# Kernel tuning notes

Hardware: AMD Instinct MI355X
Metric: run time of the kernel (lower is better)

## Reference

```python
import jax, jax.numpy as jnp
import numpy as np

N, B, E = 10000, 4, 160000
C_IN, C_OUT, C_E = 64, 64, 16


def _mk_params(key, c_in, c_out, c_e):
    ks = jax.random.split(key, 8)
    s = 0.1
    return dict(
        w_n=jax.random.normal(ks[0], (c_in, c_out), jnp.float32) * s,
        w_e=jax.random.normal(ks[1], (c_e, c_out), jnp.float32) * s,
        q=jax.random.normal(ks[2], (c_out, c_out), jnp.float32) * s,
        k=jax.random.normal(ks[3], (c_out, c_out), jnp.float32) * s,
        aw=jax.random.normal(ks[4], (3 * c_out, 1), jnp.float32) * s,
        ab=jax.random.normal(ks[5], (1,), jnp.float32) * s,
        ow=jax.random.normal(ks[6], (2 * c_out, c_out), jnp.float32) * s,
        ob=jax.random.normal(ks[7], (c_out,), jnp.float32) * s,
    )


def setup_inputs() -> dict:
    key = jax.random.key(0)
    kx, ke, ka, k1, k2 = jax.random.split(key, 5)
    inp = {
        'X': jax.random.normal(kx, (N, B, C_IN), jnp.float32),
        'edge_index': jax.random.randint(ke, (2, E), 0, N, jnp.int32),
        'edge_attr': jax.random.normal(ka, (E, C_E), jnp.float32),
    }
    p1 = _mk_params(k1, C_IN, C_OUT, C_E)
    p2 = _mk_params(k2, C_OUT, C_OUT, C_E)
    for name, v in p1.items():
        inp[name + '1'] = v
    for name, v in p2.items():
        inp[name + '2'] = v
    return inp


def egnn_conv(x, edge_index, edge_attr, w_n, w_e, q, k, aw, ab, ow, ob, n_nodes):
    # x: [N,B,Cin]; edge_attr: [E,Ce]
    xp = x @ w_n                         # [N,B,C]
    ea = edge_attr @ w_e                 # [E,C]
    src, dst = edge_index[0], edge_index[1]
    xj = xp[src]                         # [E,B,C] gather (source)
    xi = xp[dst]                         # [E,B,C] gather (target)
    qf = xj @ q                          # [E,B,C]
    kf = xi @ k                          # [E,B,C]
    eab = jnp.broadcast_to(ea[:, None, :], qf.shape)  # [E,B,C]
    att_feat = jnp.concatenate([qf, kf, eab], axis=-1)  # [E,B,3C]
    att = jax.nn.sigmoid(att_feat @ aw + ab)            # [E,B,1]
    gate = jax.nn.sigmoid(eab)
    msg = att * xj * gate                # [E,B,C]
    aggr = jax.ops.segment_max(msg, dst, num_segments=n_nodes)  # [N,B,C]
    aggr = jnp.where(jnp.isneginf(aggr), 0.0, aggr)  # empty segments -> 0
    out = jnp.concatenate([xp, aggr], axis=-1) @ ow + ob
    return xp + out


def reference(X, edge_index, edge_attr,
              w_n1, w_e1, q1, k1, aw1, ab1, ow1, ob1,
              w_n2, w_e2, q2, k2, aw2, ab2, ow2, ob2):
    n_nodes = X.shape[0]
    c1 = egnn_conv(X, edge_index, edge_attr, w_n1, w_e1, q1, k1, aw1, ab1, ow1, ob1, n_nodes)
    c1 = jax.nn.leaky_relu(c1, 0.01)
    c2 = egnn_conv(c1, edge_index, edge_attr, w_n2, w_e2, q2, k2, aw2, ab2, ow2, ob2, n_nodes)
    c2 = jax.nn.leaky_relu(c2, 0.01)
    return c2
```

## Files before the change

kernel.cpp:

```cpp
#include <hip/hip_runtime.h>
#include <math.h>

#define NN 10000
#define BB 4
#define EE 160000
#define CC 64
#define CE 16

static constexpr size_t OFF_XPA    = 0;
static constexpr size_t OFF_XPB    = 10240000;
static constexpr size_t OFF_SA     = 20480000;
static constexpr size_t OFF_SB     = 20640000;
static constexpr size_t OFF_VECS   = 20800000;
static constexpr size_t OFF_COUNTS = 20801280;
static constexpr size_t OFF_CURSOR = 20841280;
static constexpr size_t OFF_OFFS   = 20881280;
static constexpr size_t OFF_RECS   = 20921344;
static constexpr size_t OFF_ATT    = 22201344;

__device__ __forceinline__ float sigmoidf_(float x) {
    return 1.0f / (1.0f + __expf(-x));
}

__global__ void hist_vecs_kernel(const int* __restrict__ ei, int* __restrict__ counts,
                                 const float* __restrict__ q1, const float* __restrict__ k1,
                                 const float* __restrict__ aw1, const float* __restrict__ we1,
                                 const float* __restrict__ q2, const float* __restrict__ k2,
                                 const float* __restrict__ aw2, const float* __restrict__ we2,
                                 float* __restrict__ vecs) {
    int e = blockIdx.x * blockDim.x + threadIdx.x;
    if (e < EE) atomicAdd(&counts[ei[EE + e]], 1);
    if (blockIdx.x == 0) {
        int t = threadIdx.x;
        if (t < 64) {
            float a = 0.f, b = 0.f, c = 0.f, d = 0.f;
            for (int j = 0; j < 64; ++j) {
                a = fmaf(q1[t * 64 + j], aw1[j], a);
                b = fmaf(k1[t * 64 + j], aw1[64 + j], b);
                c = fmaf(q2[t * 64 + j], aw2[j], c);
                d = fmaf(k2[t * 64 + j], aw2[64 + j], d);
            }
            vecs[t] = a; vecs[64 + t] = b; vecs[144 + t] = c; vecs[208 + t] = d;
        }
        if (t < 16) {
            float a = 0.f, b = 0.f;
            for (int j = 0; j < 64; ++j) {
                a = fmaf(we1[t * 64 + j], aw1[128 + j], a);
                b = fmaf(we2[t * 64 + j], aw2[128 + j], b);
            }
            vecs[128 + t] = a; vecs[272 + t] = b;
        }
    }
}

__global__ void scan_kernel(const int* __restrict__ counts, int* __restrict__ offs, int n) {
    __shared__ int sm[1024];
    __shared__ int carry_s;
    int t = threadIdx.x;
    if (t == 0) carry_s = 0;
    __syncthreads();
    for (int base = 0; base < n; base += 1024) {
        int i = base + t;
        int v = (i < n) ? counts[i] : 0;
        sm[t] = v;
        __syncthreads();
        for (int off = 1; off < 1024; off <<= 1) {
            int add = (t >= off) ? sm[t - off] : 0;
            __syncthreads();
            sm[t] += add;
            __syncthreads();
        }
        int carry = carry_s;
        if (i < n) offs[i] = carry + sm[t] - v;
        __syncthreads();
        if (t == 1023) carry_s = carry + sm[1023];
        __syncthreads();
    }
    if (t == 0) offs[n] = carry_s;
}

__global__ void scatter_kernel(const int* __restrict__ ei, const int* __restrict__ offs,
                               int* __restrict__ cursor, int2* __restrict__ recs) {
    int e = blockIdx.x * blockDim.x + threadIdx.x;
    if (e >= EE) return;
    int s = ei[e], d = ei[EE + e];
    int p = atomicAdd(&cursor[d], 1);
    recs[offs[d] + p] = make_int2(s, e);
}

__global__ __launch_bounds__(256) void node_prep_kernel(
    const float* __restrict__ x,
    const float* __restrict__ w_n,
    const float* __restrict__ qa,
    const float* __restrict__ ka,
    float* __restrict__ xp,
    float* __restrict__ sa,
    float* __restrict__ sb) {
    __shared__ float w_sh[64 * 64];
    __shared__ float x_sh[4 * BB * CC];
    int t = threadIdx.x;
    for (int i = t; i < 64 * 64; i += 256) w_sh[i] = w_n[i];
    int node0 = blockIdx.x * 4;
    const float4* xg = (const float4*)(x + (size_t)node0 * BB * CC);
    ((float4*)x_sh)[t] = xg[t];
    __syncthreads();
    int wave = t >> 6, lane = t & 63;
    int node = node0 + wave;
    const float* xrow = x_sh + wave * BB * CC;
    float acc0 = 0.f, acc1 = 0.f, acc2 = 0.f, acc3 = 0.f;
    #pragma unroll 8
    for (int ci = 0; ci < 64; ++ci) {
        float w = w_sh[ci * 64 + lane];
        acc0 = fmaf(xrow[ci], w, acc0);
        acc1 = fmaf(xrow[64 + ci], w, acc1);
        acc2 = fmaf(xrow[128 + ci], w, acc2);
        acc3 = fmaf(xrow[192 + ci], w, acc3);
    }
    size_t obase = (size_t)node * BB * CC + lane;
    xp[obase] = acc0;
    xp[obase + 64] = acc1;
    xp[obase + 128] = acc2;
    xp[obase + 192] = acc3;
    float qv = qa[lane], kv = ka[lane];
    float ra0 = acc0 * qv, ra1 = acc1 * qv, ra2 = acc2 * qv, ra3 = acc3 * qv;
    float rb0 = acc0 * kv, rb1 = acc1 * kv, rb2 = acc2 * kv, rb3 = acc3 * kv;
    #pragma unroll
    for (int off = 32; off >= 1; off >>= 1) {
        ra0 += __shfl_xor(ra0, off, 64); ra1 += __shfl_xor(ra1, off, 64);
        ra2 += __shfl_xor(ra2, off, 64); ra3 += __shfl_xor(ra3, off, 64);
        rb0 += __shfl_xor(rb0, off, 64); rb1 += __shfl_xor(rb1, off, 64);
        rb2 += __shfl_xor(rb2, off, 64); rb3 += __shfl_xor(rb3, off, 64);
    }
    if (lane == 0) {
        sa[node * BB + 0] = ra0; sa[node * BB + 1] = ra1;
        sa[node * BB + 2] = ra2; sa[node * BB + 3] = ra3;
        sb[node * BB + 0] = rb0; sb[node * BB + 1] = rb1;
        sb[node * BB + 2] = rb2; sb[node * BB + 3] = rb3;
    }
}

__global__ __launch_bounds__(256) void att_kernel(
    const int* __restrict__ ei, const float* __restrict__ attr,
    const float* __restrict__ sa, const float* __restrict__ sb,
    const float* __restrict__ weav,
    const float* __restrict__ ab,
    float4* __restrict__ att) {
    int e = blockIdx.x * blockDim.x + threadIdx.x;
    if (e >= EE) return;
    int s = ei[e], d = ei[EE + e];
    const float4* ap = (const float4*)(attr + (size_t)e * CE);
    float4 a0 = ap[0], a1 = ap[1], a2 = ap[2], a3 = ap[3];
    float se = ab[0];
    se = fmaf(a0.x, weav[0], se);  se = fmaf(a0.y, weav[1], se);
    se = fmaf(a0.z, weav[2], se);  se = fmaf(a0.w, weav[3], se);
    se = fmaf(a1.x, weav[4], se);  se = fmaf(a1.y, weav[5], se);
    se = fmaf(a1.z, weav[6], se);  se = fmaf(a1.w, weav[7], se);
    se = fmaf(a2.x, weav[8], se);  se = fmaf(a2.y, weav[9], se);
    se = fmaf(a2.z, weav[10], se); se = fmaf(a2.w, weav[11], se);
    se = fmaf(a3.x, weav[12], se); se = fmaf(a3.y, weav[13], se);
    se = fmaf(a3.z, weav[14], se); se = fmaf(a3.w, weav[15], se);
    float4 sas = *(const float4*)(sa + (size_t)s * BB);
    float4 sbn = *(const float4*)(sb + (size_t)d * BB);
    float4 r;
    r.x = sigmoidf_(sas.x + sbn.x + se);
    r.y = sigmoidf_(sas.y + sbn.y + se);
    r.z = sigmoidf_(sas.z + sbn.z + se);
    r.w = sigmoidf_(sas.w + sbn.w + se);
    att[e] = r;
}

__global__ __launch_bounds__(256) void conv_out_kernel(
    const float* __restrict__ xp,
    const int2* __restrict__ recs,
    const int* __restrict__ offs,
    const float* __restrict__ attr,
    const float* __restrict__ w_e,
    const float4* __restrict__ att,
    const float* __restrict__ ow,
    const float* __restrict__ ob,
    float* __restrict__ out) {
    __shared__ float aggr_sh[4][BB * CC];
    __shared__ float xpn_sh[4][BB * CC];
    int t = threadIdx.x;
    int wave = t >> 6, lane = t & 63;
    int node = blockIdx.x * 4 + wave;

    float wec[CE];
    #pragma unroll
    for (int j = 0; j < CE; ++j) wec[j] = w_e[j * CC + lane];

    const float* xn = xp + (size_t)node * BB * CC + lane;
    float xn0 = xn[0], xn1 = xn[64], xn2 = xn[128], xn3 = xn[192];

    int o0 = offs[node], o1 = offs[node + 1];
    float m0 = -INFINITY, m1 = -INFINITY, m2 = -INFINITY, m3 = -INFINITY;

    int i = o0;
    int2 rec = (i < o1) ? recs[i] : make_int2(0, 0);
    while (i < o1) {
        int2 cur = rec;
        ++i;
        if (i < o1) rec = recs[i];
        int s = cur.x, e = cur.y;
        float4 at = att[e];
        const float4* ap = (const float4*)(attr + (size_t)e * CE);
        float4 a0 = ap[0], a1 = ap[1], a2 = ap[2], a3 = ap[3];
        float g = 0.f;
        g = fmaf(a0.x, wec[0], g);  g = fmaf(a0.y, wec[1], g);
        g = fmaf(a0.z, wec[2], g);  g = fmaf(a0.w, wec[3], g);
        g = fmaf(a1.x, wec[4], g);  g = fmaf(a1.y, wec[5], g);
        g = fmaf(a1.z, wec[6], g);  g = fmaf(a1.w, wec[7], g);
        g = fmaf(a2.x, wec[8], g);  g = fmaf(a2.y, wec[9], g);
        g = fmaf(a2.z, wec[10], g); g = fmaf(a2.w, wec[11], g);
        g = fmaf(a3.x, wec[12], g); g = fmaf(a3.y, wec[13], g);
        g = fmaf(a3.z, wec[14], g); g = fmaf(a3.w, wec[15], g);
        g = sigmoidf_(g);
        const float* xs = xp + (size_t)s * BB * CC + lane;
        float x0 = xs[0], x1 = xs[64], x2 = xs[128], x3 = xs[192];
        m0 = fmaxf(m0, at.x * x0 * g);
        m1 = fmaxf(m1, at.y * x1 * g);
        m2 = fmaxf(m2, at.z * x2 * g);
        m3 = fmaxf(m3, at.w * x3 * g);
    }
    m0 = (m0 == -INFINITY) ? 0.f : m0;
    m1 = (m1 == -INFINITY) ? 0.f : m1;
    m2 = (m2 == -INFINITY) ? 0.f : m2;
    m3 = (m3 == -INFINITY) ? 0.f : m3;

    aggr_sh[wave][0 * CC + lane] = m0; aggr_sh[wave][1 * CC + lane] = m1;
    aggr_sh[wave][2 * CC + lane] = m2; aggr_sh[wave][3 * CC + lane] = m3;
    xpn_sh[wave][0 * CC + lane] = xn0; xpn_sh[wave][1 * CC + lane] = xn1;
    xpn_sh[wave][2 * CC + lane] = xn2; xpn_sh[wave][3 * CC + lane] = xn3;
    __syncthreads();

    const float* xr = xpn_sh[wave];
    const float* ar = aggr_sh[wave];
    float o0f = 0.f, o1f = 0.f, o2f = 0.f, o3f = 0.f;
    #pragma unroll 4
    for (int ci = 0; ci < 64; ++ci) {
        float wa = ow[ci * 64 + lane];
        float wb = ow[(64 + ci) * 64 + lane];
        o0f = fmaf(xr[ci], wa, o0f);
        o1f = fmaf(xr[CC + ci], wa, o1f);
        o2f = fmaf(xr[2 * CC + ci], wa, o2f);
        o3f = fmaf(xr[3 * CC + ci], wa, o3f);
        o0f = fmaf(ar[ci], wb, o0f);
        o1f = fmaf(ar[CC + ci], wb, o1f);
        o2f = fmaf(ar[2 * CC + ci], wb, o2f);
        o3f = fmaf(ar[3 * CC + ci], wb, o3f);
    }
    float obv = ob[lane];
    float r0 = xn0 + o0f + obv;
    float r1 = xn1 + o1f + obv;
    float r2 = xn2 + o2f + obv;
    float r3 = xn3 + o3f + obv;
    r0 = (r0 > 0.f) ? r0 : 0.01f * r0;
    r1 = (r1 > 0.f) ? r1 : 0.01f * r1;
    r2 = (r2 > 0.f) ? r2 : 0.01f * r2;
    r3 = (r3 > 0.f) ? r3 : 0.01f * r3;
    float* op = out + (size_t)node * BB * CC + lane;
    op[0] = r0; op[64] = r1; op[128] = r2; op[192] = r3;
}

extern "C" void kernel_launch(void* const* d_in, const int* in_sizes, int n_in,
                              void* d_out, int out_size, void* d_ws, size_t ws_size,
                              hipStream_t stream) {
    const float* X    = (const float*)d_in[0];
    const int*   ei   = (const int*)d_in[1];
    const float* attr = (const float*)d_in[2];
    const float* w_n1 = (const float*)d_in[3];
    const float* w_e1 = (const float*)d_in[4];
    const float* q1   = (const float*)d_in[5];
    const float* k1   = (const float*)d_in[6];
    const float* aw1  = (const float*)d_in[7];
    const float* ab1  = (const float*)d_in[8];
    const float* ow1  = (const float*)d_in[9];
    const float* ob1  = (const float*)d_in[10];
    const float* w_n2 = (const float*)d_in[11];
    const float* w_e2 = (const float*)d_in[12];
    const float* q2   = (const float*)d_in[13];
    const float* k2   = (const float*)d_in[14];
    const float* aw2  = (const float*)d_in[15];
    const float* ab2  = (const float*)d_in[16];
    const float* ow2  = (const float*)d_in[17];
    const float* ob2  = (const float*)d_in[18];
    float* out = (float*)d_out;

    char* ws = (char*)d_ws;
    float*  xpA    = (float*)(ws + OFF_XPA);
    float*  xpB    = (float*)(ws + OFF_XPB);
    float*  sa     = (float*)(ws + OFF_SA);
    float*  sb     = (float*)(ws + OFF_SB);
    float*  vecs   = (float*)(ws + OFF_VECS);
    int*    counts = (int*)(ws + OFF_COUNTS);
    int*    cursor = (int*)(ws + OFF_CURSOR);
    int*    offs   = (int*)(ws + OFF_OFFS);
    int2*   recs   = (int2*)(ws + OFF_RECS);
    float4* att    = (float4*)(ws + OFF_ATT);

    hipMemsetAsync(counts, 0, 2 * NN * sizeof(int), stream);
    hist_vecs_kernel<<<EE / 256, 256, 0, stream>>>(ei, counts, q1, k1, aw1, w_e1,
                                                   q2, k2, aw2, w_e2, vecs);
    scan_kernel<<<1, 1024, 0, stream>>>(counts, offs, NN);
    scatter_kernel<<<EE / 256, 256, 0, stream>>>(ei, offs, cursor, recs);

    node_prep_kernel<<<NN / 4, 256, 0, stream>>>(X, w_n1, vecs + 0, vecs + 64, xpA, sa, sb);
    att_kernel<<<EE / 256, 256, 0, stream>>>(ei, attr, sa, sb, vecs + 128, ab1, att);
    conv_out_kernel<<<NN / 4, 256, 0, stream>>>(xpA, recs, offs, attr, w_e1, att,
                                                ow1, ob1, xpB);
    node_prep_kernel<<<NN / 4, 256, 0, stream>>>(xpB, w_n2, vecs + 144, vecs + 208, xpA, sa, sb);
    att_kernel<<<EE / 256, 256, 0, stream>>>(ei, attr, sa, sb, vecs + 272, ab2, att);
    conv_out_kernel<<<NN / 4, 256, 0, stream>>>(xpA, recs, offs, attr, w_e2, att,
                                                ow2, ob2, out);
}
```

Before: 312.8 us.

## Interleave batch into per-channel float4 layout, split aggregation from output GEMM, shuffle-based scan

Node features are now stored channel-major with the four batch values packed together, so each lane fetches a source node's features in one float4 load during the gather-max. The fused conv_out kernel is split into an aggregation kernel that writes to a new workspace buffer and a separate output projection kernel. This adds an extra round trip through global memory and an extra launch per layer. The single-block scan now uses wavefront shuffles in place of a shared-memory Hillis-Steele loop, which cuts the number of barriers.

```diff
diff --git a/kernel.cpp b/kernel.cpp
--- a/kernel.cpp
+++ b/kernel.cpp
@@ -9,14 +9,15 @@
 
 static constexpr size_t OFF_XPA    = 0;
 static constexpr size_t OFF_XPB    = 10240000;
-static constexpr size_t OFF_SA     = 20480000;
-static constexpr size_t OFF_SB     = 20640000;
-static constexpr size_t OFF_VECS   = 20800000;
-static constexpr size_t OFF_COUNTS = 20801280;
-static constexpr size_t OFF_CURSOR = 20841280;
-static constexpr size_t OFF_OFFS   = 20881280;
-static constexpr size_t OFF_RECS   = 20921344;
-static constexpr size_t OFF_ATT    = 22201344;
+static constexpr size_t OFF_AGG    = 20480000;
+static constexpr size_t OFF_SA     = 30720000;
+static constexpr size_t OFF_SB     = 30880000;
+static constexpr size_t OFF_VECS   = 31040000;
+static constexpr size_t OFF_COUNTS = 31041280;
+static constexpr size_t OFF_CURSOR = 31081280;
+static constexpr size_t OFF_OFFS   = 31121280;
+static constexpr size_t OFF_RECS   = 31161344;
+static constexpr size_t OFF_ATT    = 32441344;
 
 __device__ __forceinline__ float sigmoidf_(float x) {
     return 1.0f / (1.0f + __expf(-x));
@@ -54,29 +55,43 @@
 }
 
 __global__ void scan_kernel(const int* __restrict__ counts, int* __restrict__ offs, int n) {
-    __shared__ int sm[1024];
-    __shared__ int carry_s;
+    __shared__ int wsum[16];
+    __shared__ int carry_sh;
     int t = threadIdx.x;
-    if (t == 0) carry_s = 0;
+    int lane = t & 63, wid = t >> 6;
+    if (t == 0) carry_sh = 0;
     __syncthreads();
     for (int base = 0; base < n; base += 1024) {
         int i = base + t;
         int v = (i < n) ? counts[i] : 0;
-        sm[t] = v;
+        int x = v;
+        #pragma unroll
+        for (int d = 1; d < 64; d <<= 1) {
+            int y = __shfl_up(x, d, 64);
+            if (lane >= d) x += y;
+        }
+        if (lane == 63) wsum[wid] = x;
         __syncthreads();
-        for (int off = 1; off < 1024; off <<= 1) {
-            int add = (t >= off) ? sm[t - off] : 0;
-            __syncthreads();
-            sm[t] += add;
-            __syncthreads();
+        if (wid == 0 && lane < 16) {
+            int s = wsum[lane];
+            int y2 = s;
+            #pragma unroll
+            for (int d = 1; d < 16; d <<= 1) {
+                int z = __shfl_up(y2, d, 16);
+                if (lane >= d) y2 += z;
+            }
+            wsum[lane] = y2;
         }
-        int carry = carry_s;
-        if (i < n) offs[i] = carry + sm[t] - v;
         __syncthreads();
-        if (t == 1023) carry_s = carry + sm[1023];
+        int waveExcl = (wid == 0) ? 0 : wsum[wid - 1];
+        int carry = carry_sh;
+        if (i < n) offs[i] = carry + waveExcl + x - v;
+        int total = wsum[15];
         __syncthreads();
-    }
-    if (t == 0) offs[n] = carry_s;
+        if (t == 0) carry_sh = carry + total;
+        __syncthreads();
+    }
+    if (threadIdx.x == 0) offs[n] = carry_sh;
 }
 
 __global__ void scatter_kernel(const int* __restrict__ ei, const int* __restrict__ offs,
@@ -88,12 +103,13 @@
     recs[offs[d] + p] = make_int2(s, e);
 }
 
+template <bool IN_T>
 __global__ __launch_bounds__(256) void node_prep_kernel(
     const float* __restrict__ x,
     const float* __restrict__ w_n,
     const float* __restrict__ qa,
     const float* __restrict__ ka,
-    float* __restrict__ xp,
+    float* __restrict__ xp_t,
     float* __restrict__ sa,
     float* __restrict__ sb) {
     __shared__ float w_sh[64 * 64];
@@ -111,16 +127,17 @@
     #pragma unroll 8
     for (int ci = 0; ci < 64; ++ci) {
         float w = w_sh[ci * 64 + lane];
-        acc0 = fmaf(xrow[ci], w, acc0);
-        acc1 = fmaf(xrow[64 + ci], w, acc1);
-        acc2 = fmaf(xrow[128 + ci], w, acc2);
-        acc3 = fmaf(xrow[192 + ci], w, acc3);
-    }
-    size_t obase = (size_t)node * BB * CC + lane;
-    xp[obase] = acc0;
-    xp[obase + 64] = acc1;
-    xp[obase + 128] = acc2;
-    xp[obase + 192] = acc3;
+        float x0 = IN_T ? xrow[ci * 4 + 0] : xrow[ci];
+        float x1 = IN_T ? xrow[ci * 4 + 1] : xrow[64 + ci];
+        float x2 = IN_T ? xrow[ci * 4 + 2] : xrow[128 + ci];
+        float x3 = IN_T ? xrow[ci * 4 + 3] : xrow[192 + ci];
+        acc0 = fmaf(x0, w, acc0);
+        acc1 = fmaf(x1, w, acc1);
+        acc2 = fmaf(x2, w, acc2);
+        acc3 = fmaf(x3, w, acc3);
+    }
+    float4 st; st.x = acc0; st.y = acc1; st.z = acc2; st.w = acc3;
+    *(float4*)(xp_t + (size_t)node * 256 + lane * 4) = st;
     float qv = qa[lane], kv = ka[lane];
     float ra0 = acc0 * qv, ra1 = acc1 * qv, ra2 = acc2 * qv, ra3 = acc3 * qv;
     float rb0 = acc0 * kv, rb1 = acc1 * kv, rb2 = acc2 * kv, rb3 = acc3 * kv;
@@ -169,18 +186,14 @@
     att[e] = r;
 }
 
-__global__ __launch_bounds__(256) void conv_out_kernel(
-    const float* __restrict__ xp,
+__global__ __launch_bounds__(256) void aggr_kernel(
+    const float* __restrict__ xp_t,
     const int2* __restrict__ recs,
     const int* __restrict__ offs,
     const float* __restrict__ attr,
     const float* __restrict__ w_e,
     const float4* __restrict__ att,
-    const float* __restrict__ ow,
-    const float* __restrict__ ob,
-    float* __restrict__ out) {
-    __shared__ float aggr_sh[4][BB * CC];
-    __shared__ float xpn_sh[4][BB * CC];
+    float* __restrict__ aggr_t) {
     int t = threadIdx.x;
     int wave = t >> 6, lane = t & 63;
     int node = blockIdx.x * 4 + wave;
@@ -188,9 +201,6 @@
     float wec[CE];
     #pragma unroll
     for (int j = 0; j < CE; ++j) wec[j] = w_e[j * CC + lane];
-
-    const float* xn = xp + (size_t)node * BB * CC + lane;
-    float xn0 = xn[0], xn1 = xn[64], xn2 = xn[128], xn3 = xn[192];
 
     int o0 = offs[node], o1 = offs[node + 1];
     float m0 = -INFINITY, m1 = -INFINITY, m2 = -INFINITY, m3 = -INFINITY;
@@ -203,6 +213,7 @@
         if (i < o1) rec = recs[i];
         int s = cur.x, e = cur.y;
         float4 at = att[e];
+        float4 xv = *(const float4*)(xp_t + (size_t)s * 256 + lane * 4);
         const float4* ap = (const float4*)(attr + (size_t)e * CE);
         float4 a0 = ap[0], a1 = ap[1], a2 = ap[2], a3 = ap[3];
         float g = 0.f;
@@ -215,51 +226,72 @@
         g = fmaf(a3.x, wec[12], g); g = fmaf(a3.y, wec[13], g);
         g = fmaf(a3.z, wec[14], g); g = fmaf(a3.w, wec[15], g);
         g = sigmoidf_(g);
-        const float* xs = xp + (size_t)s * BB * CC + lane;
-        float x0 = xs[0], x1 = xs[64], x2 = xs[128], x3 = xs[192];
-        m0 = fmaxf(m0, at.x * x0 * g);
-        m1 = fmaxf(m1, at.y * x1 * g);
-        m2 = fmaxf(m2, at.z * x2 * g);
-        m3 = fmaxf(m3, at.w * x3 * g);
+        m0 = fmaxf(m0, at.x * xv.x * g);
+        m1 = fmaxf(m1, at.y * xv.y * g);
+        m2 = fmaxf(m2, at.z * xv.z * g);
+        m3 = fmaxf(m3, at.w * xv.w * g);
     }
     m0 = (m0 == -INFINITY) ? 0.f : m0;
     m1 = (m1 == -INFINITY) ? 0.f : m1;
     m2 = (m2 == -INFINITY) ? 0.f : m2;
     m3 = (m3 == -INFINITY) ? 0.f : m3;
-
-    aggr_sh[wave][0 * CC + lane] = m0; aggr_sh[wave][1 * CC + lane] = m1;
-    aggr_sh[wave][2 * CC + lane] = m2; aggr_sh[wave][3 * CC + lane] = m3;
-    xpn_sh[wave][0 * CC + lane] = xn0; xpn_sh[wave][1 * CC + lane] = xn1;
-    xpn_sh[wave][2 * CC + lane] = xn2; xpn_sh[wave][3 * CC + lane] = xn3;
+    float4 st; st.x = m0; st.y = m1; st.z = m2; st.w = m3;
+    *(float4*)(aggr_t + (size_t)node * 256 + lane * 4) = st;
+}
+
+template <bool WRITE_T>
+__global__ __launch_bounds__(256) void out_kernel(
+    const float* __restrict__ xp_t,
+    const float* __restrict__ aggr_t,
+    const float* __restrict__ ow,
+    const float* __restrict__ ob,
+    float* __restrict__ out) {
+    __shared__ float xs[4][BB * CC];
+    __shared__ float as_[4][BB * CC];
+    int t = threadIdx.x;
+    int wave = t >> 6, lane = t & 63;
+    int node = blockIdx.x * 4 + wave;
+
+    float4 xv = *(const float4*)(xp_t + (size_t)node * 256 + lane * 4);
+    float4 av = *(const float4*)(aggr_t + (size_t)node * 256 + lane * 4);
+    xs[wave][0 * 64 + lane] = xv.x; xs[wave][1 * 64 + lane] = xv.y;
+    xs[wave][2 * 64 + lane] = xv.z; xs[wave][3 * 64 + lane] = xv.w;
+    as_[wave][0 * 64 + lane] = av.x; as_[wave][1 * 64 + lane] = av.y;
+    as_[wave][2 * 64 + lane] = av.z; as_[wave][3 * 64 + lane] = av.w;
     __syncthreads();
 
-    const float* xr = xpn_sh[wave];
-    const float* ar = aggr_sh[wave];
+    const float* xr = xs[wave];
+    const float* ar = as_[wave];
     float o0f = 0.f, o1f = 0.f, o2f = 0.f, o3f = 0.f;
     #pragma unroll 4
     for (int ci = 0; ci < 64; ++ci) {
         float wa = ow[ci * 64 + lane];
         float wb = ow[(64 + ci) * 64 + lane];
         o0f = fmaf(xr[ci], wa, o0f);
-        o1f = fmaf(xr[CC + ci], wa, o1f);
-        o2f = fmaf(xr[2 * CC + ci], wa, o2f);
-        o3f = fmaf(xr[3 * CC + ci], wa, o3f);
+        o1f = fmaf(xr[64 + ci], wa, o1f);
+        o2f = fmaf(xr[128 + ci], wa, o2f);
+        o3f = fmaf(xr[192 + ci], wa, o3f);
         o0f = fmaf(ar[ci], wb, o0f);
-        o1f = fmaf(ar[CC + ci], wb, o1f);
-        o2f = fmaf(ar[2 * CC + ci], wb, o2f);
-        o3f = fmaf(ar[3 * CC + ci], wb, o3f);
+        o1f = fmaf(ar[64 + ci], wb, o1f);
+        o2f = fmaf(ar[128 + ci], wb, o2f);
+        o3f = fmaf(ar[192 + ci], wb, o3f);
     }
     float obv = ob[lane];
-    float r0 = xn0 + o0f + obv;
-    float r1 = xn1 + o1f + obv;
-    float r2 = xn2 + o2f + obv;
-    float r3 = xn3 + o3f + obv;
+    float r0 = xv.x + o0f + obv;
+    float r1 = xv.y + o1f + obv;
+    float r2 = xv.z + o2f + obv;
+    float r3 = xv.w + o3f + obv;
     r0 = (r0 > 0.f) ? r0 : 0.01f * r0;
     r1 = (r1 > 0.f) ? r1 : 0.01f * r1;
     r2 = (r2 > 0.f) ? r2 : 0.01f * r2;
     r3 = (r3 > 0.f) ? r3 : 0.01f * r3;
-    float* op = out + (size_t)node * BB * CC + lane;
-    op[0] = r0; op[64] = r1; op[128] = r2; op[192] = r3;
+    if (WRITE_T) {
+        float4 st; st.x = r0; st.y = r1; st.z = r2; st.w = r3;
+        *(float4*)(out + (size_t)node * 256 + lane * 4) = st;
+    } else {
+        float* op = out + (size_t)node * 256 + lane;
+        op[0] = r0; op[64] = r1; op[128] = r2; op[192] = r3;
+    }
 }
 
 extern "C" void kernel_launch(void* const* d_in, const int* in_sizes, int n_in,
@@ -289,6 +321,7 @@
     char* ws = (char*)d_ws;
     float*  xpA    = (float*)(ws + OFF_XPA);
     float*  xpB    = (float*)(ws + OFF_XPB);
+    float*  agg    = (float*)(ws + OFF_AGG);
     float*  sa     = (float*)(ws + OFF_SA);
     float*  sb     = (float*)(ws + OFF_SB);
     float*  vecs   = (float*)(ws + OFF_VECS);
@@ -304,12 +337,15 @@
     scan_kernel<<<1, 1024, 0, stream>>>(counts, offs, NN);
     scatter_kernel<<<EE / 256, 256, 0, stream>>>(ei, offs, cursor, recs);
 
-    node_prep_kernel<<<NN / 4, 256, 0, stream>>>(X, w_n1, vecs + 0, vecs + 64, xpA, sa, sb);
+    node_prep_kernel<false><<<NN / 4, 256, 0, stream>>>(X, w_n1, vecs + 0, vecs + 64,
+                                                        xpA, sa, sb);
     att_kernel<<<EE / 256, 256, 0, stream>>>(ei, attr, sa, sb, vecs + 128, ab1, att);
-    conv_out_kernel<<<NN / 4, 256, 0, stream>>>(xpA, recs, offs, attr, w_e1, att,
-                                                ow1, ob1, xpB);
-    node_prep_kernel<<<NN / 4, 256, 0, stream>>>(xpB, w_n2, vecs + 144, vecs + 208, xpA, sa, sb);
+    aggr_kernel<<<NN / 4, 256, 0, stream>>>(xpA, recs, offs, attr, w_e1, att, agg);
+    out_kernel<true><<<NN / 4, 256, 0, stream>>>(xpA, agg, ow1, ob1, xpB);
+
+    node_prep_kernel<true><<<NN / 4, 256, 0, stream>>>(xpB, w_n2, vecs + 144, vecs + 208,
+                                                       xpA, sa, sb);
     att_kernel<<<EE / 256, 256, 0, stream>>>(ei, attr, sa, sb, vecs + 272, ab2, att);
-    conv_out_kernel<<<NN / 4, 256, 0, stream>>>(xpA, recs, offs, attr, w_e2, att,
-                                                ow2, ob2, out);
-}
+    aggr_kernel<<<NN / 4, 256, 0, stream>>>(xpA, recs, offs, attr, w_e2, att, agg);
+    out_kernel<false><<<NN / 4, 256, 0, stream>>>(xpA, agg, ow2, ob2, out);
+}
```

Result: no change. 316.8 us (+1.3%).
